# Performance work log

Hardware: AMD Instinct MI355X
Metric: run time of the kernel (lower is better)

## Reference

```python
import jax, jax.numpy as jnp
import numpy as np

B, T, C = 4, 2048, 768
H, D = 12, 64          # num heads, head size
MLP = 3072
EPS = 1e-6
SCALE = C ** (-0.5)    # NOTE: source scales by n_embd**-0.5, not head_size**-0.5


def setup_inputs() -> dict:
    key = jax.random.key(0)
    ks = jax.random.split(key, 12)
    s = 0.02
    return {
        "x":     jax.random.normal(ks[0], (B, T, C), jnp.float32),
        "Wq":    jax.random.normal(ks[1], (H, C, D), jnp.float32) * s,
        "Wk":    jax.random.normal(ks[2], (H, C, D), jnp.float32) * s,
        "Wv":    jax.random.normal(ks[3], (H, C, D), jnp.float32) * s,
        "Wo":    jax.random.normal(ks[4], (H * D, C), jnp.float32) * s,
        "bo":    jnp.zeros((C,), jnp.float32),
        "ln1_g": jnp.ones((C,), jnp.float32),
        "ln1_b": jnp.zeros((C,), jnp.float32),
        "ln2_g": jnp.ones((C,), jnp.float32),
        "ln2_b": jnp.zeros((C,), jnp.float32),
        "W1":    jax.random.normal(ks[5], (C, MLP), jnp.float32) * s,
        "b1":    jnp.zeros((MLP,), jnp.float32),
        "W2":    jax.random.normal(ks[6], (MLP, C), jnp.float32) * s,
        "b2":    jnp.zeros((C,), jnp.float32),
    }


def _ln(x, g, b):
    mu = jnp.mean(x, axis=-1, keepdims=True)
    var = jnp.var(x, axis=-1, keepdims=True)
    return (x - mu) * jax.lax.rsqrt(var + EPS) * g + b


def reference(x, Wq, Wk, Wv, Wo, bo, ln1_g, ln1_b, ln2_g, ln2_b, W1, b1, W2, b2):
    xn = _ln(x, ln1_g, ln1_b)
    # batched per-head projections: [B,T,C] x [H,C,D] -> [B,H,T,D]
    q = jnp.einsum("btc,hcd->bhtd", xn, Wq)
    k = jnp.einsum("btc,hcd->bhtd", xn, Wk)
    v = jnp.einsum("btc,hcd->bhtd", xn, Wv)
    wei = jnp.einsum("bhtd,bhsd->bhts", q, k) * SCALE  # [B,H,T,T]
    wei = jax.nn.softmax(wei, axis=-1)
    attn = jnp.einsum("bhts,bhsd->bhtd", wei, v)
    # concat heads along feature dim (head order preserved)
    attn = attn.transpose(0, 2, 1, 3).reshape(B, T, H * D)
    sa = attn @ Wo + bo
    x2 = sa + x                      # residual 1 (dropout = identity in eval)
    y = _ln(x2, ln2_g, ln2_b)
    y = jax.nn.gelu(y @ W1 + b1, approximate=False) @ W2 + b2
    return x2 + y                    # residual 2
```

## Files before the change

### kernel.cpp

```cpp
#include <hip/hip_runtime.h>
#include <hip/hip_bf16.h>
#include <cstdint>
#include <cmath>

#define B_ 4
#define T_ 2048
#define C_ 768
#define H_ 12
#define D_ 64
#define MLP_ 3072
#define BT_ (B_*T_)

typedef __hip_bfloat16 hbf;
typedef __bf16 bf16_t;
typedef bf16_t bf16x8 __attribute__((ext_vector_type(8)));
typedef bf16_t bf16x4 __attribute__((ext_vector_type(4)));
typedef float f32x4 __attribute__((ext_vector_type(4)));

static __device__ __forceinline__ void load_lds16(const void* g, void* l) {
    __builtin_amdgcn_global_load_lds(
        (const __attribute__((address_space(1))) unsigned int*)g,
        (__attribute__((address_space(3))) unsigned int*)l, 16, 0, 0);
}

__global__ __launch_bounds__(256) void transpose_pack(
    const float* __restrict__ src, hbf* __restrict__ dst, int R, int S)
{
    __shared__ float tl[64 * 65];
    src += (size_t)blockIdx.z * R * S;
    dst += (size_t)blockIdx.z * R * S;
    const int r0 = blockIdx.y * 64, s0 = blockIdx.x * 64;
    const int c = threadIdx.x & 63, q = threadIdx.x >> 6;
#pragma unroll
    for (int j = 0; j < 16; ++j) {
        int r = q + j * 4;
        tl[r * 65 + c] = src[(size_t)(r0 + r) * S + s0 + c];
    }
    __syncthreads();
#pragma unroll
    for (int j = 0; j < 16; ++j) {
        int s = q + j * 4;
        dst[(size_t)(s0 + s) * R + r0 + c] = __float2bfloat16(tl[c * 65 + s]);
    }
}

__global__ __launch_bounds__(256) void pack_qkv3(
    const float* __restrict__ Wq, const float* __restrict__ Wk,
    const float* __restrict__ Wv, hbf* __restrict__ WqkT)
{
    __shared__ float tl[64 * 65];
    const int z = blockIdx.z;
    const int mtx = z / 12, head = z - mtx * 12;
    const float* src = (mtx == 0 ? Wq : mtx == 1 ? Wk : Wv) + (size_t)head * 49152;
    hbf* dst = WqkT + (size_t)z * 49152;
    const int r0 = blockIdx.y * 64;
    const int c = threadIdx.x & 63, q = threadIdx.x >> 6;
#pragma unroll
    for (int j = 0; j < 16; ++j) {
        int r = q + j * 4;
        tl[r * 65 + c] = src[(size_t)(r0 + r) * 64 + c];
    }
    __syncthreads();
#pragma unroll
    for (int j = 0; j < 16; ++j) {
        int s = q + j * 4;
        dst[(size_t)s * 768 + r0 + c] = __float2bfloat16(tl[c * 65 + s]);
    }
}

template<typename TI>
__global__ __launch_bounds__(256) void ln_kernel(
    const TI* __restrict__ x, const float* __restrict__ g,
    const float* __restrict__ bb, hbf* __restrict__ out)
{
    __shared__ float red[8];
    const int row = blockIdx.x;
    const TI* xr = x + (size_t)row * C_;
    const int t = threadIdx.x;
    float v0, v1, v2;
    if constexpr (__is_same(TI, float)) {
        v0 = xr[t]; v1 = xr[t + 256]; v2 = xr[t + 512];
    } else {
        v0 = __bfloat162float(xr[t]);
        v1 = __bfloat162float(xr[t + 256]);
        v2 = __bfloat162float(xr[t + 512]);
    }
    float s = v0 + v1 + v2;
    float s2 = v0 * v0 + v1 * v1 + v2 * v2;
#pragma unroll
    for (int m = 1; m < 64; m <<= 1) {
        s  += __shfl_xor(s,  m, 64);
        s2 += __shfl_xor(s2, m, 64);
    }
    if ((t & 63) == 0) { red[t >> 6] = s; red[4 + (t >> 6)] = s2; }
    __syncthreads();
    float S  = red[0] + red[1] + red[2] + red[3];
    float S2 = red[4] + red[5] + red[6] + red[7];
    float mu  = S * (1.0f / C_);
    float var = S2 * (1.0f / C_) - mu * mu;
    float inv = rsqrtf(var + 1e-6f);
    hbf* orow = out + (size_t)row * C_;
    orow[t]       = __float2bfloat16((v0 - mu) * inv * g[t]       + bb[t]);
    orow[t + 256] = __float2bfloat16((v1 - mu) * inv * g[t + 256] + bb[t + 256]);
    orow[t + 512] = __float2bfloat16((v2 - mu) * inv * g[t + 512] + bb[t + 512]);
}

template<int EPI, int TN>
__global__ __launch_bounds__(256, (TN == 64) ? 4 : 3) void gemm_kernel(
    const hbf* __restrict__ A, const hbf* __restrict__ Bt,
    float* __restrict__ outF, hbf* __restrict__ outH,
    const float* __restrict__ bias, const float* __restrict__ residF,
    const hbf* __restrict__ residH,
    int M, int N, int K,
    hbf* __restrict__ qb, hbf* __restrict__ kb, hbf* __restrict__ vt,
    float scale, int gx)
{
    constexpr int AM = (TN == 128) ? 4 : 2;
    constexpr int NB_B = (TN == 128) ? 4 : 2;
    __shared__ hbf sA[128 * 64];
    __shared__ hbf sB[TN * 64];
    const int tid = threadIdx.x;
    const int lane = tid & 63;
    const int wid = tid >> 6;
    const int lr = lane & 15, hg = lane >> 4;
    const int bid = blockIdx.x, nwg = gridDim.x;
    const int wg = (bid & 7) * (nwg >> 3) + (bid >> 3);
    const int bx = wg % gx, by = wg / gx;
    const int row0 = by * 128;
    const int col0 = bx * TN;
    const int wrow = (TN == 128) ? (wid >> 1) * 64 : wid * 32;
    const int wcol = (TN == 128) ? (wid & 1) * 64 : 0;

    f32x4 acc[AM][4] = {};

    int offG[4];
    const int Kb = K * 2;
#pragma unroll
    for (int i = 0; i < 4; ++i) {
        int c = tid + i * 256;
        offG[i] = (c >> 3) * Kb + (((c & 7) ^ ((c >> 3) & 7)) << 4);
    }
    const char* gA = (const char*)(A + (size_t)row0 * K);
    const char* gB = (const char*)(Bt + (size_t)col0 * K);

    auto stage = [&](int kt) {
        const int kb2 = kt * 128;
#pragma unroll
        for (int i = 0; i < 4; ++i)
            load_lds16(gA + (size_t)(offG[i] + kb2), (char*)sA + i * 4096 + wid * 1024);
#pragma unroll
        for (int i = 0; i < NB_B; ++i)
            load_lds16(gB + (size_t)(offG[i] + kb2), (char*)sB + i * 4096 + wid * 1024);
    };

    const int NK = K >> 6;
    stage(0);
    for (int kt = 0; kt < NK; ++kt) {
        __syncthreads();
#pragma unroll
        for (int kf = 0; kf < 2; ++kf) {
            const int sl = ((kf * 4 + hg) ^ (lr & 7)) << 4;
            bf16x8 af[AM], bfr[4];
#pragma unroll
            for (int m = 0; m < AM; ++m)
                af[m] = *(const bf16x8*)((const char*)sA + (wrow + m * 16 + lr) * 128 + sl);
#pragma unroll
            for (int n = 0; n < 4; ++n)
                bfr[n] = *(const bf16x8*)((const char*)sB + (wcol + n * 16 + lr) * 128 + sl);
#pragma unroll
            for (int m = 0; m < AM; ++m)
#pragma unroll
                for (int n = 0; n < 4; ++n)
                    acc[m][n] = __builtin_amdgcn_mfma_f32_16x16x32_bf16(af[m], bfr[n], acc[m][n], 0, 0, 0);
        }
        __syncthreads();
        if (kt + 1 < NK) stage(kt + 1);
    }

#pragma unroll
    for (int m = 0; m < AM; ++m) {
#pragma unroll
        for (int n = 0; n < 4; ++n) {
            const int colc = col0 + wcol + n * 16 + lr;
            const int rowb = row0 + wrow + m * 16 + hg * 4;
            if constexpr (EPI == 3) {
                if (colc >= 2 * C_) {
                    bf16x4 w;
#pragma unroll
                    for (int j = 0; j < 4; ++j) w[j] = (bf16_t)acc[m][n][j];
                    *(bf16x4*)(vt + (size_t)(colc - 2 * C_) * BT_ + rowb) = w;
                    continue;
                }
            }
#pragma unroll
            for (int j = 0; j < 4; ++j) {
                int row = rowb + j;
                int col = colc;
                float v = acc[m][n][j];
                if constexpr (EPI == 0) {
                    outH[(size_t)row * N + col] = __float2bfloat16(v);
                } else if constexpr (EPI == 2) {
                    float tt = v + bias[col];
                    float ge = 0.5f * tt * (1.0f + erff(tt * 0.70710678118654752f));
                    outH[(size_t)row * N + col] = __float2bfloat16(ge);
                } else if constexpr (EPI == 3) {
                    int typ = col / C_;
                    int rr = col - typ * C_;
                    int h = rr >> 6, d = rr & 63;
                    int b = row >> 11, t = row & (T_ - 1);
                    size_t bh = (size_t)b * H_ + h;
                    if (typ == 0) qb[(bh * T_ + t) * D_ + d] = __float2bfloat16(v * scale);
                    else          kb[(bh * T_ + t) * D_ + d] = __float2bfloat16(v);
                } else if constexpr (EPI == 4) {
                    outH[(size_t)row * N + col] =
                        __float2bfloat16(v + bias[col] + residF[(size_t)row * N + col]);
                } else {
                    outF[(size_t)row * N + col] =
                        v + bias[col] + __bfloat162float(residH[(size_t)row * N + col]);
                }
            }
        }
    }
}

__global__ __launch_bounds__(256, 3) void attn_kernel(
    const hbf* __restrict__ qg, const hbf* __restrict__ kg,
    const hbf* __restrict__ vg, hbf* __restrict__ outA)
{
    __shared__ hbf sK0[64 * 64], sK1[64 * 64];
    __shared__ hbf sV0[64 * 64], sV1[64 * 64];
    __shared__ hbf sP[4 * 32 * 64];
    const int tid = threadIdx.x, lane = tid & 63, wid = tid >> 6;
    const int lr = lane & 15, hg = lane >> 4;
    const int wg = (blockIdx.x & 7) * 96 + (blockIdx.x >> 3);
    const int bh = wg >> 4;
    const int b = bh / H_, h = bh - b * H_;
    const int wr0 = (wg & 15) * 128 + wid * 32;
    const hbf* qbh = qg + (size_t)bh * T_ * D_;
    const hbf* kbh = kg + (size_t)bh * T_ * D_;
    const hbf* vbh = vg + (size_t)h * 64 * BT_ + (size_t)b * T_;

    bf16x8 a_q[2][2];
#pragma unroll
    for (int m = 0; m < 2; ++m)
#pragma unroll
        for (int kf = 0; kf < 2; ++kf)
            a_q[m][kf] = *(const bf16x8*)(qbh + (size_t)(wr0 + m * 16 + lr) * D_ + kf * 32 + hg * 8);

    bf16x8 vone;
#pragma unroll
    for (int i = 0; i < 8; ++i) vone[i] = (bf16_t)1.0f;

    f32x4 o[2][4] = {};
    f32x4 lden[2] = {};
    float mreg[2] = {-3e38f, -3e38f};

    int offK[2], offV[2];
#pragma unroll
    for (int i = 0; i < 2; ++i) {
        int c = tid + i * 256;
        int sw = ((c & 7) ^ ((c >> 3) & 7)) << 4;
        offK[i] = (c >> 3) * 128 + sw;
        offV[i] = (c >> 3) * (BT_ * 2) + sw;
    }
    hbf* sPw = sP + wid * (32 * 64);
    const int sl0 = ((0 * 4 + hg) ^ (lr & 7)) << 4;
    const int sl1 = ((1 * 4 + hg) ^ (lr & 7)) << 4;
    const int bcast = hg * 20;

    auto stage = [&](int itn, hbf* sKd, hbf* sVd) {
        const char* kp = (const char*)kbh + (size_t)itn * 8192;
        const char* vp = (const char*)vbh + (size_t)itn * 128;
#pragma unroll
        for (int i = 0; i < 2; ++i) {
            load_lds16(kp + offK[i], (char*)sKd + i * 4096 + wid * 1024);
            load_lds16(vp + offV[i], (char*)sVd + i * 4096 + wid * 1024);
        }
    };

    auto tile = [&](const hbf* sKc, const hbf* sVc) {
        f32x4 st[4][2] = {};
        __builtin_amdgcn_s_setprio(1);
#pragma unroll
        for (int kf = 0; kf < 2; ++kf) {
            const int sl = kf ? sl1 : sl0;
#pragma unroll
            for (int n = 0; n < 4; ++n) {
                bf16x8 ak = *(const bf16x8*)((const char*)sKc + (n * 16 + lr) * 128 + sl);
                st[n][0] = __builtin_amdgcn_mfma_f32_16x16x32_bf16(ak, a_q[0][kf], st[n][0], 0, 0, 0);
                st[n][1] = __builtin_amdgcn_mfma_f32_16x16x32_bf16(ak, a_q[1][kf], st[n][1], 0, 0, 0);
            }
        }
        __builtin_amdgcn_s_setprio(0);

#pragma unroll
        for (int m = 0; m < 2; ++m) {
            f32x4 mx = st[0][m];
            mx[0] = fmaxf(mx[0], st[1][m][0]); mx[1] = fmaxf(mx[1], st[1][m][1]);
            mx[2] = fmaxf(mx[2], st[1][m][2]); mx[3] = fmaxf(mx[3], st[1][m][3]);
            f32x4 my = st[2][m];
            my[0] = fmaxf(my[0], st[3][m][0]); my[1] = fmaxf(my[1], st[3][m][1]);
            my[2] = fmaxf(my[2], st[3][m][2]); my[3] = fmaxf(my[3], st[3][m][3]);
            float t01 = fmaxf(fmaxf(mx[0], my[0]), fmaxf(mx[1], my[1]));
            float t23 = fmaxf(fmaxf(mx[2], my[2]), fmaxf(mx[3], my[3]));
            float t = fmaxf(t01, t23);
            t = fmaxf(t, __shfl_xor(t, 16, 64));
            t = fmaxf(t, __shfl_xor(t, 32, 64));
            if (__any(t - mreg[m] > 11.5415603f)) {
                float nm = fmaxf(mreg[m], t);
                float fac = __builtin_amdgcn_exp2f(mreg[m] - nm);
                mreg[m] = nm;
                float fb[4];
#pragma unroll
                for (int j = 0; j < 4; ++j)
                    fb[j] = __shfl(fac, bcast + j, 64);
#pragma unroll
                for (int j = 0; j < 4; ++j) {
                    lden[m][j] *= fb[j];
#pragma unroll
                    for (int nd = 0; nd < 4; ++nd)
                        o[m][nd][j] *= fb[j];
                }
            }
            const int r = m * 16 + lr;
#pragma unroll
            for (int n = 0; n < 4; ++n) {
                float p0 = __builtin_amdgcn_exp2f(st[n][m][0] - mreg[m]);
                float p1 = __builtin_amdgcn_exp2f(st[n][m][1] - mreg[m]);
                float p2 = __builtin_amdgcn_exp2f(st[n][m][2] - mreg[m]);
                float p3 = __builtin_amdgcn_exp2f(st[n][m][3] - mreg[m]);
                bf16x4 w;
                w[0] = (bf16_t)p0; w[1] = (bf16_t)p1; w[2] = (bf16_t)p2; w[3] = (bf16_t)p3;
                *(bf16x4*)((char*)sPw + r * 128 +
                           (((n * 2 + (hg >> 1)) ^ (r & 7)) << 4) + ((hg & 1) * 8)) = w;
            }
        }

        __builtin_amdgcn_s_setprio(1);
#pragma unroll
        for (int kf = 0; kf < 2; ++kf) {
            const int sl = kf ? sl1 : sl0;
            bf16x8 ap0 = *(const bf16x8*)((const char*)sPw + lr * 128 + sl);
            bf16x8 ap1 = *(const bf16x8*)((const char*)sPw + (16 + lr) * 128 + sl);
            lden[0] = __builtin_amdgcn_mfma_f32_16x16x32_bf16(ap0, vone, lden[0], 0, 0, 0);
            lden[1] = __builtin_amdgcn_mfma_f32_16x16x32_bf16(ap1, vone, lden[1], 0, 0, 0);
#pragma unroll
            for (int nd = 0; nd < 4; ++nd) {
                bf16x8 bv = *(const bf16x8*)((const char*)sVc + (nd * 16 + lr) * 128 + sl);
                o[0][nd] = __builtin_amdgcn_mfma_f32_16x16x32_bf16(ap0, bv, o[0][nd], 0, 0, 0);
                o[1][nd] = __builtin_amdgcn_mfma_f32_16x16x32_bf16(ap1, bv, o[1][nd], 0, 0, 0);
            }
        }
        __builtin_amdgcn_s_setprio(0);
    };

    const int NT = T_ / 64;
    stage(0, sK0, sV0);
    __syncthreads();
    for (int it = 0; it < NT; it += 2) {
        stage(it + 1, sK1, sV1);
        tile(sK0, sV0);
        __syncthreads();
        if (it + 2 < NT) stage(it + 2, sK0, sV0);
        tile(sK1, sV1);
        __syncthreads();
    }

#pragma unroll
    for (int m = 0; m < 2; ++m) {
        f32x4 rinv;
#pragma unroll
        for (int j = 0; j < 4; ++j) rinv[j] = 1.0f / lden[m][j];
#pragma unroll
        for (int nd = 0; nd < 4; ++nd)
#pragma unroll
            for (int j = 0; j < 4; ++j) {
                int row = wr0 + m * 16 + hg * 4 + j;
                int col = nd * 16 + lr;
                outA[((size_t)(b * T_ + row)) * C_ + h * D_ + col] =
                    __float2bfloat16(o[m][nd][j] * rinv[j]);
            }
    }
}

extern "C" void kernel_launch(void* const* d_in, const int* in_sizes, int n_in,
                              void* d_out, int out_size, void* d_ws, size_t ws_size,
                              hipStream_t stream)
{
    const float* x    = (const float*)d_in[0];
    const float* Wq   = (const float*)d_in[1];
    const float* Wk   = (const float*)d_in[2];
    const float* Wv   = (const float*)d_in[3];
    const float* Wo   = (const float*)d_in[4];
    const float* bo   = (const float*)d_in[5];
    const float* ln1g = (const float*)d_in[6];
    const float* ln1b = (const float*)d_in[7];
    const float* ln2g = (const float*)d_in[8];
    const float* ln2b = (const float*)d_in[9];
    const float* W1   = (const float*)d_in[10];
    const float* b1   = (const float*)d_in[11];
    const float* W2   = (const float*)d_in[12];
    const float* b2   = (const float*)d_in[13];
    float* out = (float*)d_out;
    char* ws = (char*)d_ws;

    hbf*  xn    = (hbf*)(ws + 0);
    hbf*  WqkT  = (hbf*)(ws + 12582912);
    hbf*  qb    = (hbf*)(ws + 16121856);
    hbf*  kb    = (hbf*)(ws + 28704768);
    hbf*  vT    = (hbf*)(ws + 41287680);
    hbf*  h1    = (hbf*)(ws + 0);
    hbf*  attnB = (hbf*)(ws + 53870592);
    hbf*  yln   = (hbf*)(ws + 53870592);
    hbf*  x2b   = (hbf*)(ws + 66453504);
    hbf*  WoT   = (hbf*)(ws + 91619328);
    hbf*  W1T   = (hbf*)(ws + 92798976);
    hbf*  W2T   = (hbf*)(ws + 97517568);

    const float SCALE2 = 0.036084391824351615f * 1.4426950408889634f;

    pack_qkv3<<<dim3(1, 12, 36), 256, 0, stream>>>(Wq, Wk, Wv, WqkT);
    transpose_pack<<<dim3(12, 12, 1), 256, 0, stream>>>(Wo, WoT, 768, 768);
    transpose_pack<<<dim3(48, 12, 1), 256, 0, stream>>>(W1, W1T, 768, 3072);
    transpose_pack<<<dim3(12, 48, 1), 256, 0, stream>>>(W2, W2T, 3072, 768);
    ln_kernel<float><<<8192, 256, 0, stream>>>(x, ln1g, ln1b, xn);
    gemm_kernel<3,128><<<1152, 256, 0, stream>>>(xn, WqkT, nullptr, nullptr, nullptr, nullptr,
        nullptr, 8192, 2304, 768, qb, kb, vT, SCALE2, 18);
    attn_kernel<<<768, 256, 0, stream>>>(qb, kb, vT, attnB);
    gemm_kernel<4,64><<<768, 256, 0, stream>>>(attnB, WoT, nullptr, x2b, bo, x,
        nullptr, 8192, 768, 768, nullptr, nullptr, nullptr, 1.0f, 12);
    ln_kernel<hbf><<<8192, 256, 0, stream>>>(x2b, ln2g, ln2b, yln);
    gemm_kernel<2,128><<<1536, 256, 0, stream>>>(yln, W1T, nullptr, h1, b1, nullptr,
        nullptr, 8192, 3072, 768, nullptr, nullptr, nullptr, 1.0f, 24);
    gemm_kernel<5,64><<<768, 256, 0, stream>>>(h1, W2T, out, nullptr, b2, nullptr,
        x2b, 8192, 768, 3072, nullptr, nullptr, nullptr, 1.0f, 12);
}
```

Measured before the change: 277.2 us.

## Vectorize layernorm, use tanh-approx GELU, and permlane row-max in attention

```diff
diff --git a/kernel.cpp b/kernel.cpp
--- a/kernel.cpp
+++ b/kernel.cpp
@@ -69,40 +69,45 @@
 }
 
 template<typename TI>
-__global__ __launch_bounds__(256) void ln_kernel(
+__global__ __launch_bounds__(192) void ln_kernel(
     const TI* __restrict__ x, const float* __restrict__ g,
     const float* __restrict__ bb, hbf* __restrict__ out)
 {
-    __shared__ float red[8];
+    __shared__ float red[6];
     const int row = blockIdx.x;
-    const TI* xr = x + (size_t)row * C_;
     const int t = threadIdx.x;
-    float v0, v1, v2;
+    float v[4];
     if constexpr (__is_same(TI, float)) {
-        v0 = xr[t]; v1 = xr[t + 256]; v2 = xr[t + 512];
+        const float4 xv = *(const float4*)(x + (size_t)row * C_ + t * 4);
+        v[0] = xv.x; v[1] = xv.y; v[2] = xv.z; v[3] = xv.w;
     } else {
-        v0 = __bfloat162float(xr[t]);
-        v1 = __bfloat162float(xr[t + 256]);
-        v2 = __bfloat162float(xr[t + 512]);
-    }
-    float s = v0 + v1 + v2;
-    float s2 = v0 * v0 + v1 * v1 + v2 * v2;
+        bf16x4 xv = *(const bf16x4*)((const bf16_t*)x + (size_t)row * C_ + t * 4);
+#pragma unroll
+        for (int k = 0; k < 4; ++k) v[k] = (float)xv[k];
+    }
+    float s = 0.0f, s2 = 0.0f;
+#pragma unroll
+    for (int k = 0; k < 4; ++k) { s += v[k]; s2 += v[k] * v[k]; }
 #pragma unroll
     for (int m = 1; m < 64; m <<= 1) {
         s  += __shfl_xor(s,  m, 64);
         s2 += __shfl_xor(s2, m, 64);
     }
-    if ((t & 63) == 0) { red[t >> 6] = s; red[4 + (t >> 6)] = s2; }
+    if ((t & 63) == 0) { red[t >> 6] = s; red[3 + (t >> 6)] = s2; }
     __syncthreads();
-    float S  = red[0] + red[1] + red[2] + red[3];
-    float S2 = red[4] + red[5] + red[6] + red[7];
+    float S  = red[0] + red[1] + red[2];
+    float S2 = red[3] + red[4] + red[5];
     float mu  = S * (1.0f / C_);
     float var = S2 * (1.0f / C_) - mu * mu;
     float inv = rsqrtf(var + 1e-6f);
-    hbf* orow = out + (size_t)row * C_;
-    orow[t]       = __float2bfloat16((v0 - mu) * inv * g[t]       + bb[t]);
-    orow[t + 256] = __float2bfloat16((v1 - mu) * inv * g[t + 256] + bb[t + 256]);
-    orow[t + 512] = __float2bfloat16((v2 - mu) * inv * g[t + 512] + bb[t + 512]);
+    const float4 gv = *(const float4*)(g  + t * 4);
+    const float4 bv = *(const float4*)(bb + t * 4);
+    bf16x4 o4;
+    o4[0] = (bf16_t)((v[0] - mu) * inv * gv.x + bv.x);
+    o4[1] = (bf16_t)((v[1] - mu) * inv * gv.y + bv.y);
+    o4[2] = (bf16_t)((v[2] - mu) * inv * gv.z + bv.z);
+    o4[3] = (bf16_t)((v[3] - mu) * inv * gv.w + bv.w);
+    *(bf16x4*)((bf16_t*)out + (size_t)row * C_ + t * 4) = o4;
 }
 
 template<int EPI, int TN>
@@ -201,7 +206,10 @@
                     outH[(size_t)row * N + col] = __float2bfloat16(v);
                 } else if constexpr (EPI == 2) {
                     float tt = v + bias[col];
-                    float ge = 0.5f * tt * (1.0f + erff(tt * 0.70710678118654752f));
+                    float t3 = tt * tt * tt;
+                    float z = fminf(fmaf(t3, 0.1029423372f, 2.3021141876f * tt), 126.0f);
+                    float e = __builtin_amdgcn_exp2f(z);
+                    float ge = tt * e * __builtin_amdgcn_rcpf(e + 1.0f);
                     outH[(size_t)row * N + col] = __float2bfloat16(ge);
                 } else if constexpr (EPI == 3) {
                     int typ = col / C_;
@@ -293,6 +301,7 @@
         }
         __builtin_amdgcn_s_setprio(0);
 
+        float tm[2];
 #pragma unroll
         for (int m = 0; m < 2; ++m) {
             f32x4 mx = st[0][m];
@@ -303,9 +312,23 @@
             my[2] = fmaxf(my[2], st[3][m][2]); my[3] = fmaxf(my[3], st[3][m][3]);
             float t01 = fmaxf(fmaxf(mx[0], my[0]), fmaxf(mx[1], my[1]));
             float t23 = fmaxf(fmaxf(mx[2], my[2]), fmaxf(mx[3], my[3]));
-            float t = fmaxf(t01, t23);
-            t = fmaxf(t, __shfl_xor(t, 16, 64));
-            t = fmaxf(t, __shfl_xor(t, 32, 64));
+            tm[m] = fmaxf(t01, t23);
+        }
+        {
+            float a0 = tm[0], b0 = tm[0], a1 = tm[1], b1 = tm[1];
+            asm volatile("v_permlane32_swap_b32 %0, %1" : "+v"(a0), "+v"(b0));
+            asm volatile("v_permlane32_swap_b32 %0, %1" : "+v"(a1), "+v"(b1));
+            a0 = fmaxf(a0, b0);
+            a1 = fmaxf(a1, b1);
+            float s0 = __shfl_xor(a0, 16, 64);
+            float s1 = __shfl_xor(a1, 16, 64);
+            tm[0] = fmaxf(a0, s0);
+            tm[1] = fmaxf(a1, s1);
+        }
+
+#pragma unroll
+        for (int m = 0; m < 2; ++m) {
+            const float t = tm[m];
             if (__any(t - mreg[m] > 11.5415603f)) {
                 float nm = fmaxf(mreg[m], t);
                 float fac = __builtin_amdgcn_exp2f(mreg[m] - nm);
@@ -423,13 +446,13 @@
     transpose_pack<<<dim3(12, 12, 1), 256, 0, stream>>>(Wo, WoT, 768, 768);
     transpose_pack<<<dim3(48, 12, 1), 256, 0, stream>>>(W1, W1T, 768, 3072);
     transpose_pack<<<dim3(12, 48, 1), 256, 0, stream>>>(W2, W2T, 3072, 768);
-    ln_kernel<float><<<8192, 256, 0, stream>>>(x, ln1g, ln1b, xn);
+    ln_kernel<float><<<8192, 192, 0, stream>>>(x, ln1g, ln1b, xn);
     gemm_kernel<3,128><<<1152, 256, 0, stream>>>(xn, WqkT, nullptr, nullptr, nullptr, nullptr,
         nullptr, 8192, 2304, 768, qb, kb, vT, SCALE2, 18);
     attn_kernel<<<768, 256, 0, stream>>>(qb, kb, vT, attnB);
     gemm_kernel<4,64><<<768, 256, 0, stream>>>(attnB, WoT, nullptr, x2b, bo, x,
         nullptr, 8192, 768, 768, nullptr, nullptr, nullptr, 1.0f, 12);
-    ln_kernel<hbf><<<8192, 256, 0, stream>>>(x2b, ln2g, ln2b, yln);
+    ln_kernel<hbf><<<8192, 192, 0, stream>>>(x2b, ln2g, ln2b, yln);
     gemm_kernel<2,128><<<1536, 256, 0, stream>>>(yln, W1T, nullptr, h1, b1, nullptr,
         nullptr, 8192, 3072, 768, nullptr, nullptr, nullptr, 1.0f, 24);
     gemm_kernel<5,64><<<768, 256, 0, stream>>>(h1, W2T, out, nullptr, b2, nullptr,
```

Result: faster. 267.4 us (-3.5%).
